# Performance work log

Hardware: AMD Instinct MI355X
Metric: run time of the kernel (lower is better)

## Reference

```python
import jax, jax.numpy as jnp
import numpy as np

N_NODES = 50000
N_EDGES = 1600000
HID = 128
NF = 128
NG = 50
NL = 6
CUTOFF = 20.0
NSEG = 64


def _ssp(x):
    # ShiftedSoftplus: softplus(x) - log(2)
    return jax.nn.softplus(x) - jnp.log(2.0).astype(x.dtype)


def setup_inputs() -> dict:
    key = jax.random.key(0)
    ks = jax.random.split(key, 24)
    s = 0.05
    inp = {
        "h": jax.random.normal(ks[0], (N_NODES, HID), dtype=jnp.float32),
        "pos": jax.random.normal(ks[1], (N_NODES, 3), dtype=jnp.float32),
        "edge_index": jax.random.randint(ks[2], (2, N_EDGES), 0, N_NODES, dtype=jnp.int64),
        "batch": jnp.sort(jax.random.randint(ks[3], (N_NODES,), 0, NSEG, dtype=jnp.int64)),
        # per-interaction-block params, stacked over NL layers (weights in [in, out] layout)
        "mlp_w1": jax.random.normal(ks[4], (NL, NG, NF), dtype=jnp.float32) * s,
        "mlp_b1": jnp.zeros((NL, NF), dtype=jnp.float32),
        "mlp_w2": jax.random.normal(ks[5], (NL, NF, NF), dtype=jnp.float32) * s,
        "mlp_b2": jnp.zeros((NL, NF), dtype=jnp.float32),
        "conv_lin1_w": jax.random.normal(ks[6], (NL, HID, NF), dtype=jnp.float32) * s,  # no bias
        "conv_lin2_w": jax.random.normal(ks[7], (NL, NF, HID), dtype=jnp.float32) * s,
        "conv_lin2_b": jnp.zeros((NL, HID), dtype=jnp.float32),
        "lin_w": jax.random.normal(ks[8], (NL, HID, HID), dtype=jnp.float32) * s,
        "lin_b": jnp.zeros((NL, HID), dtype=jnp.float32),
        # readout head
        "out1_w": jax.random.normal(ks[9], (HID, HID // 2), dtype=jnp.float32) * s,
        "out1_b": jnp.zeros((HID // 2,), dtype=jnp.float32),
        "out2_w": jax.random.normal(ks[10], (HID // 2, 1), dtype=jnp.float32) * s,
        "out2_b": jnp.zeros((1,), dtype=jnp.float32),
    }
    return inp


def reference(h, pos, edge_index, batch, mlp_w1, mlp_b1, mlp_w2, mlp_b2,
              conv_lin1_w, conv_lin2_w, conv_lin2_b, lin_w, lin_b,
              out1_w, out1_b, out2_w, out2_b):
    src = edge_index[0]  # j (messages gathered here)
    dst = edge_index[1]  # i (messages aggregated here)
    n = h.shape[0]

    # edge distances from positions (RadiusInteractionGraph.forward)
    diff = pos[src] - pos[dst]                       # [E, 3]
    d = jnp.sqrt(jnp.sum(diff * diff, axis=-1))      # [E]

    # GaussianSmearing
    offset = jnp.linspace(0.0, CUTOFF, NG, dtype=h.dtype)
    coeff = -0.5 / (offset[1] - offset[0]) ** 2
    edge_attr = jnp.exp(coeff * (d[:, None] - offset[None, :]) ** 2)  # [E, NG]

    # cosine cutoff envelope
    C = 0.5 * (jnp.cos(d * jnp.pi / CUTOFF) + 1.0)   # [E]

    for l in range(NL):
        # continuous filter from edge features
        W = _ssp(edge_attr @ mlp_w1[l] + mlp_b1[l]) @ mlp_w2[l] + mlp_b2[l]  # [E, NF]
        W = W * C[:, None]
        # CFConv: lin1 -> gather x_j -> * W -> scatter-add -> lin2
        hx = h @ conv_lin1_w[l]                       # [N, NF]
        msg = hx[src] * W                             # [E, NF]
        agg = jax.ops.segment_sum(msg, dst, num_segments=n)  # [N, NF]
        hc = agg @ conv_lin2_w[l] + conv_lin2_b[l]    # [N, HID]
        # InteractionBlock: act then lin, residual add in SchNet.forward
        h = h + (_ssp(hc) @ lin_w[l] + lin_b[l])

    # readout head
    o = _ssp(h @ out1_w + out1_b) @ out2_w + out2_b   # [N, 1]
    # 'add' readout over molecules
    return jax.ops.segment_sum(o, batch, num_segments=NSEG)  # [NSEG, 1]
```

## Files before the change

kernel.cpp:

```cpp
#include <hip/hip_runtime.h>
#include <math.h>

#define N_NODES 50000
#define N_EDGES 1600000
#define HID 128
#define NF 128
#define NG 50
#define NL 6
#define NSEG 64
#define TAB2 4096
#define CUTOFF 20.0f
#define LOG2F_ 0.6931471805599453f

typedef unsigned short u16;
typedef __attribute__((ext_vector_type(8))) short short8;
typedef __attribute__((ext_vector_type(8))) unsigned short ushort8;
typedef __attribute__((ext_vector_type(4))) float f32x4;

__device__ __forceinline__ float ssp(float x){
  float sp = fmaxf(x, 0.f) + log1pf(expf(-fabsf(x)));
  return sp - LOG2F_;
}
__device__ __forceinline__ float b2f(u16 u){
  unsigned v = ((unsigned)u) << 16; float f; __builtin_memcpy(&f, &v, 4); return f;
}
__device__ __forceinline__ u16 f2b(float f){
  unsigned u; __builtin_memcpy(&u, &f, 4);
  u += 0x7FFFu + ((u >> 16) & 1u);
  return (u16)(u >> 16);
}
__device__ __forceinline__ int swz(int row, int colb){
  return row*256 + (colb ^ ((row & 15) << 4));
}

__global__ __launch_bounds__(256) void k_hist(const int* __restrict__ ei_dst,
                                              int* __restrict__ deg){
  int e4 = blockIdx.x*blockDim.x + threadIdx.x;
  if (e4 < N_EDGES/4){
    int4 d = ((const int4*)ei_dst)[e4];
    atomicAdd(&deg[d.x], 1);
    atomicAdd(&deg[d.y], 1);
    atomicAdd(&deg[d.z], 1);
    atomicAdd(&deg[d.w], 1);
  }
}

__global__ __launch_bounds__(1024) void k_scan1(const int* __restrict__ deg,
                                                int* __restrict__ row_start,
                                                int* __restrict__ bsum){
  int i = blockIdx.x*1024 + threadIdx.x;
  int lane = threadIdx.x & 63, w = threadIdx.x >> 6;
  int x = (i < N_NODES) ? deg[i] : 0;
  int v = x;
  #pragma unroll
  for (int off = 1; off < 64; off <<= 1){
    int t = __shfl_up(v, off);
    if (lane >= off) v += t;
  }
  __shared__ int ws[16];
  if (lane == 63) ws[w] = v;
  __syncthreads();
  if (w == 0 && lane < 16){
    int t = ws[lane];
    #pragma unroll
    for (int off = 1; off < 16; off <<= 1){
      int u = __shfl_up(t, off);
      if (lane >= off) t += u;
    }
    ws[lane] = t;
  }
  __syncthreads();
  int woff = (w > 0) ? ws[w-1] : 0;
  if (i < N_NODES) row_start[i] = woff + v - x;
  if (threadIdx.x == 1023) bsum[blockIdx.x] = woff + v;
}

__global__ __launch_bounds__(1024) void k_scan2(const int* __restrict__ bsum,
                                                int* __restrict__ row_start){
  __shared__ int boff_s;
  if (threadIdx.x < 64){
    int lane = threadIdx.x;
    int acc = 0;
    for (int b = lane; b < blockIdx.x; b += 64) acc += bsum[b];
    #pragma unroll
    for (int off = 32; off >= 1; off >>= 1) acc += __shfl_xor(acc, off);
    if (lane == 0) boff_s = acc;
  }
  __syncthreads();
  int i = blockIdx.x*1024 + threadIdx.x;
  if (i < N_NODES) row_start[i] += boff_s;
  if (i == 0) row_start[N_NODES] = N_EDGES;
}

__global__ __launch_bounds__(256) void k_scatter(const int* __restrict__ ei,
                                                 const float* __restrict__ pos,
                                                 const int* __restrict__ row_start,
                                                 int* __restrict__ cursor,
                                                 unsigned* __restrict__ csr_pack){
  const float INV_STEP = (TAB2 - 1) / CUTOFF;
  for (int e = blockIdx.x*blockDim.x + threadIdx.x; e < N_EDGES; e += gridDim.x*blockDim.x){
    int s = ei[e], t = ei[N_EDGES + e];
    float dx = pos[3*s]   - pos[3*t];
    float dy = pos[3*s+1] - pos[3*t+1];
    float dz = pos[3*s+2] - pos[3*t+2];
    float d = sqrtf(dx*dx + dy*dy + dz*dz);
    int j = (int)(d * INV_STEP + 0.5f);
    if (j > TAB2 - 1) j = TAB2 - 1;
    int slot = atomicAdd(&cursor[t], 1);
    int p = row_start[t] + slot;
    __builtin_nontemporal_store(((unsigned)j << 16) | (unsigned)s, &csr_pack[p]);
  }
}

__global__ __launch_bounds__(128) void k_table(const float* __restrict__ w1, const float* __restrict__ b1,
                                               const float* __restrict__ w2, const float* __restrict__ b2,
                                               u16* __restrict__ tab){
  int l = blockIdx.x / TAB2, j = blockIdx.x % TAB2;
  int tid = threadIdx.x;
  float d = j * (CUTOFF / (TAB2 - 1));
  __shared__ float ea[NG];
  __shared__ float sbuf[NF];
  if (tid < NG){
    const float gstep = CUTOFF / (NG - 1);
    const float coeff = -0.5f / (gstep * gstep);
    float u = d - tid * gstep;
    ea[tid] = expf(coeff * u * u);
  }
  __syncthreads();
  float z = b1[l*NF + tid];
  for (int k = 0; k < NG; k++) z += ea[k] * w1[(l*NG + k)*NF + tid];
  sbuf[tid] = ssp(z);
  __syncthreads();
  float W = b2[l*NF + tid];
  for (int k = 0; k < NF; k++) W += sbuf[k] * w2[(l*NF + k)*NF + tid];
  float C = 0.5f * (cosf(d * (float)M_PI / CUTOFF) + 1.f);
  tab[((size_t)l*TAB2 + j)*NF + tid] = f2b(W * C);
}

__global__ __launch_bounds__(128) void k_wconv(const float* __restrict__ w, u16* __restrict__ wT){
  int m = blockIdx.x >> 7, o = blockIdx.x & 127;
  int i = threadIdx.x;
  wT[((size_t)m*128 + o)*128 + i] = f2b(w[((size_t)m*128 + i)*128 + o]);
}
__global__ __launch_bounds__(128) void k_wconv64(const float* __restrict__ w, u16* __restrict__ wT){
  int o = blockIdx.x;
  int i = threadIdx.x;
  wT[o*128 + i] = f2b(w[i*64 + o]);
}

__global__ __launch_bounds__(256) void k_lin1m(const float* __restrict__ h,
                                               const u16* __restrict__ w1T,
                                               u16* __restrict__ hxb){
  int tid = threadIdx.x;
  int wv = tid >> 6, l = tid & 63;
  int n0 = blockIdx.x * 64 + wv * 16;
  if (n0 >= N_NODES) return;
  int li = l & 15, lh = l >> 4;
  __shared__ u16 tiles[4][16*128];
  char* tb = (char*)&tiles[wv][0];

  short8 a[4];
  #pragma unroll
  for (int kc = 0; kc < 4; kc++){
    const float* p = &h[(size_t)(n0 + li)*HID + kc*32 + lh*8];
    union { short8 v; u16 u[8]; } t;
    #pragma unroll
    for (int e = 0; e < 8; e++) t.u[e] = f2b(p[e]);
    a[kc] = t.v;
  }
  #pragma unroll
  for (int fc = 0; fc < 8; fc++){
    f32x4 acc = {0.f,0.f,0.f,0.f};
    #pragma unroll
    for (int kc = 0; kc < 4; kc++){
      short8 b = *(const short8*)&w1T[(size_t)(fc*16 + li)*HID + kc*32 + lh*8];
      acc = __builtin_amdgcn_mfma_f32_16x16x32_bf16(a[kc], b, acc, 0, 0, 0);
    }
    #pragma unroll
    for (int r = 0; r < 4; r++)
      *(u16*)(tb + swz(lh*4 + r, fc*32 + li*2)) = f2b(acc[r]);
  }
  #pragma unroll
  for (int g = 0; g < 4; g++){
    int row = g*4 + lh;
    short8 v = *(const short8*)(tb + swz(row, li*16));
    *(short8*)&hxb[(size_t)(n0 + row)*NF + li*8] = v;
  }
}

__global__ __launch_bounds__(256) void k_edgeagg(const int* __restrict__ row_start,
                                                 const unsigned* __restrict__ csr_pack,
                                                 const u16* __restrict__ tab_l,
                                                 const u16* __restrict__ hxb,
                                                 u16* __restrict__ aggb){
  int wave = threadIdx.x >> 6, lane = threadIdx.x & 63;
  int i = blockIdx.x * 4 + wave;
  int li = lane & 15, g = lane >> 4;
  int rs = row_start[i], re = row_start[i + 1];
  float acc0[8], acc1[8];
  #pragma unroll
  for (int r = 0; r < 8; r++){ acc0[r] = 0.f; acc1[r] = 0.f; }
  for (int p = rs + g; p < re; p += 8){
    int p1 = p + 4;
    bool ok1 = p1 < re;
    unsigned v0 = csr_pack[p];
    unsigned v1 = ok1 ? csr_pack[p1] : 0u;
    int s0 = (int)(v0 & 0xFFFFu), j0 = (int)(v0 >> 16);
    ushort8 hv0 = *(const ushort8*)&hxb[(size_t)s0 * NF + li*8];
    ushort8 wv0 = *(const ushort8*)&tab_l[(size_t)j0 * NF + li*8];
    if (ok1){
      int s1 = (int)(v1 & 0xFFFFu), j1 = (int)(v1 >> 16);
      ushort8 hv1 = *(const ushort8*)&hxb[(size_t)s1 * NF + li*8];
      ushort8 wv1 = *(const ushort8*)&tab_l[(size_t)j1 * NF + li*8];
      #pragma unroll
      for (int r = 0; r < 8; r++)
        acc1[r] += b2f(hv1[r]) * b2f(wv1[r]);
    }
    #pragma unroll
    for (int r = 0; r < 8; r++)
      acc0[r] += b2f(hv0[r]) * b2f(wv0[r]);
  }
  #pragma unroll
  for (int r = 0; r < 8; r++){
    float a = acc0[r] + acc1[r];
    a += __shfl_xor(a, 16);
    a += __shfl_xor(a, 32);
    acc0[r] = a;
  }
  if (g == 0){
    union { short8 v; u16 u[8]; } o;
    #pragma unroll
    for (int r = 0; r < 8; r++) o.u[r] = f2b(acc0[r]);
    *(short8*)&aggb[(size_t)i * NF + li*8] = o.v;
  }
}

__global__ __launch_bounds__(256) void k_nodefuse(const u16* __restrict__ aggb,
                                                  const u16* __restrict__ w2T, const float* __restrict__ b2b,
                                                  const u16* __restrict__ lT,  const float* __restrict__ linb,
                                                  float* __restrict__ h,
                                                  const u16* __restrict__ w1nT,
                                                  u16* __restrict__ hxb){
  int tid = threadIdx.x;
  int wv = tid >> 6, l = tid & 63;
  int n0 = blockIdx.x * 64 + wv * 16;
  if (n0 >= N_NODES) return;
  int li = l & 15, lh = l >> 4;
  __shared__ u16 tiles[4][16*128];
  char* tb = (char*)&tiles[wv][0];

  short8 a[4];
  #pragma unroll
  for (int kc = 0; kc < 4; kc++)
    a[kc] = *(const short8*)&aggb[(size_t)(n0 + li)*NF + kc*32 + lh*8];

  #pragma unroll
  for (int fc = 0; fc < 8; fc++){
    f32x4 acc = {0.f,0.f,0.f,0.f};
    #pragma unroll
    for (int kc = 0; kc < 4; kc++){
      short8 b = *(const short8*)&w2T[(size_t)(fc*16 + li)*NF + kc*32 + lh*8];
      acc = __builtin_amdgcn_mfma_f32_16x16x32_bf16(a[kc], b, acc, 0, 0, 0);
    }
    float bias = b2b[fc*16 + li];
    #pragma unroll
    for (int r = 0; r < 4; r++){
      float s = ssp(acc[r] + bias);
      *(u16*)(tb + swz(lh*4 + r, fc*32 + li*2)) = f2b(s);
    }
  }

  short8 a2[4];
  #pragma unroll
  for (int kc = 0; kc < 4; kc++)
    a2[kc] = *(const short8*)(tb + swz(li, kc*64 + lh*16));

  #pragma unroll
  for (int fc = 0; fc < 8; fc++){
    f32x4 acc = {0.f,0.f,0.f,0.f};
    #pragma unroll
    for (int kc = 0; kc < 4; kc++){
      short8 b = *(const short8*)&lT[(size_t)(fc*16 + li)*HID + kc*32 + lh*8];
      acc = __builtin_amdgcn_mfma_f32_16x16x32_bf16(a2[kc], b, acc, 0, 0, 0);
    }
    float bias = linb[fc*16 + li];
    #pragma unroll
    for (int r = 0; r < 4; r++){
      int i = lh*4 + r;
      size_t off = (size_t)(n0 + i)*HID + fc*16 + li;
      float hn = h[off] + acc[r] + bias;
      h[off] = hn;
      if (w1nT) *(u16*)(tb + swz(i, fc*32 + li*2)) = f2b(hn);
    }
  }
  if (!w1nT) return;

  short8 a3[4];
  #pragma unroll
  for (int kc = 0; kc < 4; kc++)
    a3[kc] = *(const short8*)(tb + swz(li, kc*64 + lh*16));
  #pragma unroll
  for (int fc = 0; fc < 8; fc++){
    f32x4 acc = {0.f,0.f,0.f,0.f};
    #pragma unroll
    for (int kc = 0; kc < 4; kc++){
      short8 b = *(const short8*)&w1nT[(size_t)(fc*16 + li)*HID + kc*32 + lh*8];
      acc = __builtin_amdgcn_mfma_f32_16x16x32_bf16(a3[kc], b, acc, 0, 0, 0);
    }
    #pragma unroll
    for (int r = 0; r < 4; r++)
      *(u16*)(tb + swz(lh*4 + r, fc*32 + li*2)) = f2b(acc[r]);
  }
  #pragma unroll
  for (int g = 0; g < 4; g++){
    int row = g*4 + lh;
    short8 v = *(const short8*)(tb + swz(row, li*16));
    *(short8*)&hxb[(size_t)(n0 + row)*NF + li*8] = v;
  }
}

__global__ __launch_bounds__(256) void k_out(const float* __restrict__ h,
                                             const u16* __restrict__ o1wT, const float* __restrict__ b1,
                                             const float* __restrict__ w2, const float* __restrict__ b2,
                                             const int* __restrict__ batch, float* __restrict__ out){
  int tid = threadIdx.x;
  int wv = tid >> 6, l = tid & 63;
  int base = blockIdx.x * 64 + wv * 16;
  if (base >= N_NODES) return;
  int li = l & 15, lh = l >> 4;
  __shared__ float o_s[4][16];

  short8 a[4];
  #pragma unroll
  for (int kc = 0; kc < 4; kc++){
    const float* p = &h[(size_t)(base + li)*HID + kc*32 + lh*8];
    union { short8 v; u16 u[8]; } t;
    #pragma unroll
    for (int e = 0; e < 8; e++) t.u[e] = f2b(p[e]);
    a[kc] = t.v;
  }
  float psum[4] = {0.f,0.f,0.f,0.f};
  #pragma unroll
  for (int fc = 0; fc < 4; fc++){
    f32x4 acc = {0.f,0.f,0.f,0.f};
    #pragma unroll
    for (int kc = 0; kc < 4; kc++){
      short8 b = *(const short8*)&o1wT[(size_t)(fc*16 + li)*HID + kc*32 + lh*8];
      acc = __builtin_amdgcn_mfma_f32_16x16x32_bf16(a[kc], b, acc, 0, 0, 0);
    }
    int col = fc*16 + li;
    float bias = b1[col], w2v = w2[col];
    #pragma unroll
    for (int r = 0; r < 4; r++)
      psum[r] += ssp(acc[r] + bias) * w2v;
  }
  #pragma unroll
  for (int r = 0; r < 4; r++){
    psum[r] += __shfl_xor(psum[r], 1);
    psum[r] += __shfl_xor(psum[r], 2);
    psum[r] += __shfl_xor(psum[r], 4);
    psum[r] += __shfl_xor(psum[r], 8);
  }
  float b2v = b2[0];
  if (li == 0){
    #pragma unroll
    for (int r = 0; r < 4; r++) o_s[wv][lh*4 + r] = psum[r] + b2v;
  }
  float v = o_s[wv][li];
  int n2 = base + li;
  int seg = batch[n2];
  int segn = (li < 15) ? batch[n2 + 1] : -1;
  #pragma unroll
  for (int off = 1; off <= 8; off <<= 1){
    float vv = __shfl_up(v, off);
    int   ss = __shfl_up(seg, off);
    if (li >= off && ss == seg) v += vv;
  }
  if (l < 16 && (li == 15 || segn != seg)) atomicAdd(&out[seg], v);
}

extern "C" void kernel_launch(void* const* d_in, const int* in_sizes, int n_in,
                              void* d_out, int out_size, void* d_ws, size_t ws_size,
                              hipStream_t stream) {
  const float* h     = (const float*)d_in[0];
  const float* pos   = (const float*)d_in[1];
  const int*   ei    = (const int*)d_in[2];
  const int*   batch = (const int*)d_in[3];
  const float* mlp_w1 = (const float*)d_in[4];
  const float* mlp_b1 = (const float*)d_in[5];
  const float* mlp_w2 = (const float*)d_in[6];
  const float* mlp_b2 = (const float*)d_in[7];
  const float* cl1w  = (const float*)d_in[8];
  const float* cl2w  = (const float*)d_in[9];
  const float* cl2b  = (const float*)d_in[10];
  const float* linw  = (const float*)d_in[11];
  const float* linb  = (const float*)d_in[12];
  const float* o1w   = (const float*)d_in[13];
  const float* o1b   = (const float*)d_in[14];
  const float* o2w   = (const float*)d_in[15];
  const float* o2b   = (const float*)d_in[16];
  float* out = (float*)d_out;

  char* ws = (char*)d_ws;
  size_t off = 0;
  float* h_cur = (float*)(ws + off); off += (size_t)N_NODES*HID*4;
  u16*   aggb  = (u16*)  (ws + off); off += (size_t)N_NODES*NF*2;
  u16*   hxb   = (u16*)  (ws + off); off += (size_t)N_NODES*NF*2;
  u16*   tab   = (u16*)  (ws + off); off += (size_t)NL*TAB2*NF*2;
  u16*   w1T   = (u16*)  (ws + off); off += (size_t)NL*HID*NF*2;
  u16*   w2T   = (u16*)  (ws + off); off += (size_t)NL*NF*HID*2;
  u16*   lT    = (u16*)  (ws + off); off += (size_t)NL*HID*HID*2;
  u16*   o1wT  = (u16*)  (ws + off); off += (size_t)64*HID*2;
  unsigned* csr_pack = (unsigned*)(ws + off); off += (size_t)(N_EDGES + 16)*4;
  int* deg       = (int*)(ws + off); off += (size_t)N_NODES*4;
  int* row_start = (int*)(ws + off); off += (size_t)(N_NODES + 64)*4;
  int* cursor    = (int*)(ws + off); off += (size_t)N_NODES*4;
  int* bsum      = (int*)(ws + off); off += (size_t)64*4;

  hipMemsetAsync(out, 0, NSEG*sizeof(float), stream);
  hipMemsetAsync(deg, 0, N_NODES*sizeof(int), stream);
  hipMemsetAsync(cursor, 0, N_NODES*sizeof(int), stream);
  hipMemcpyAsync(h_cur, h, (size_t)N_NODES*HID*sizeof(float), hipMemcpyDeviceToDevice, stream);

  const int NSB = (N_NODES + 1023) / 1024;
  k_hist<<<(N_EDGES/4 + 255)/256, 256, 0, stream>>>(ei + N_EDGES, deg);
  k_scan1<<<NSB, 1024, 0, stream>>>(deg, row_start, bsum);
  k_scan2<<<NSB, 1024, 0, stream>>>(bsum, row_start);
  k_scatter<<<2048, 256, 0, stream>>>(ei, pos, row_start, cursor, csr_pack);
  k_table<<<NL*TAB2, 128, 0, stream>>>(mlp_w1, mlp_b1, mlp_w2, mlp_b2, tab);
  k_wconv<<<NL*128, 128, 0, stream>>>(cl1w, w1T);
  k_wconv<<<NL*128, 128, 0, stream>>>(cl2w, w2T);
  k_wconv<<<NL*128, 128, 0, stream>>>(linw, lT);
  k_wconv64<<<64, 128, 0, stream>>>(o1w, o1wT);

  const int NBLK = (N_NODES + 63) / 64;
  k_lin1m<<<NBLK, 256, 0, stream>>>(h_cur, w1T, hxb);
  for (int l = 0; l < NL; l++){
    k_edgeagg<<<N_NODES/4, 256, 0, stream>>>(row_start, csr_pack,
                                             tab + (size_t)l*TAB2*NF, hxb, aggb);
    const u16* w1n = (l + 1 < NL) ? (w1T + (size_t)(l+1)*HID*NF) : nullptr;
    k_nodefuse<<<NBLK, 256, 0, stream>>>(aggb, w2T + (size_t)l*NF*HID, cl2b + (size_t)l*HID,
                                         lT + (size_t)l*HID*HID, linb + (size_t)l*HID,
                                         h_cur, w1n, hxb);
  }
  k_out<<<NBLK, 256, 0, stream>>>(h_cur, o1wT, o1b, o2w, o2b, batch, out);
}
```

Baseline: 937.0 us.

## Pad CSR rows to even length and load edge pairs as 64-bit in edgeagg

Each node's CSR row is padded to an even length with a sentinel entry that points at a zero-weight table row. The aggregation kernel can then fetch two packed edge indices per lane with one 64-bit nontemporal load, prefetch the next pair, and drop the per-pair bounds branch. The bf16 multiply-accumulate now works on packed 32-bit words with shifts and masks. In exchange it adds a padding kernel, a larger CSR buffer and a few wasted gathers for the padded entries.

```diff
diff --git a/kernel.cpp b/kernel.cpp
--- a/kernel.cpp
+++ b/kernel.cpp
@@ -11,8 +11,10 @@
 #define TAB2 4096
 #define CUTOFF 20.0f
 #define LOG2F_ 0.6931471805599453f
+#define SENTINEL 0x0FFF0000u
 
 typedef unsigned short u16;
+typedef unsigned long long u64;
 typedef __attribute__((ext_vector_type(8))) short short8;
 typedef __attribute__((ext_vector_type(8))) unsigned short ushort8;
 typedef __attribute__((ext_vector_type(4))) float f32x4;
@@ -28,6 +30,13 @@
   unsigned u; __builtin_memcpy(&u, &f, 4);
   u += 0x7FFFu + ((u >> 16) & 1u);
   return (u16)(u >> 16);
+}
+__device__ __forceinline__ float u2f(unsigned u){
+  float f; __builtin_memcpy(&f, &u, 4); return f;
+}
+__device__ __forceinline__ void fma2(unsigned hp, unsigned wp, float& a0, float& a1){
+  a0 = fmaf(u2f(hp << 16), u2f(wp << 16), a0);
+  a1 = fmaf(u2f(hp & 0xFFFF0000u), u2f(wp & 0xFFFF0000u), a1);
 }
 __device__ __forceinline__ int swz(int row, int colb){
   return row*256 + (colb ^ ((row & 15) << 4));
@@ -50,7 +59,7 @@
                                                 int* __restrict__ bsum){
   int i = blockIdx.x*1024 + threadIdx.x;
   int lane = threadIdx.x & 63, w = threadIdx.x >> 6;
-  int x = (i < N_NODES) ? deg[i] : 0;
+  int x = (i < N_NODES) ? ((deg[i] + 1) & ~1) : 0;
   int v = x;
   #pragma unroll
   for (int off = 1; off < 64; off <<= 1){
@@ -76,6 +85,7 @@
 }
 
 __global__ __launch_bounds__(1024) void k_scan2(const int* __restrict__ bsum,
+                                                const int* __restrict__ deg,
                                                 int* __restrict__ row_start){
   __shared__ int boff_s;
   if (threadIdx.x < 64){
@@ -88,8 +98,19 @@
   }
   __syncthreads();
   int i = blockIdx.x*1024 + threadIdx.x;
-  if (i < N_NODES) row_start[i] += boff_s;
-  if (i == 0) row_start[N_NODES] = N_EDGES;
+  if (i < N_NODES){
+    int r = row_start[i] + boff_s;
+    row_start[i] = r;
+    if (i == N_NODES - 1) row_start[N_NODES] = r + ((deg[i] + 1) & ~1);
+  }
+}
+
+__global__ __launch_bounds__(256) void k_pad(const int* __restrict__ deg,
+                                             const int* __restrict__ row_start,
+                                             unsigned* __restrict__ csr_pack){
+  int i = blockIdx.x*blockDim.x + threadIdx.x;
+  if (i < N_NODES && (deg[i] & 1))
+    csr_pack[row_start[i] + deg[i]] = SENTINEL;
 }
 
 __global__ __launch_bounds__(256) void k_scatter(const int* __restrict__ ei,
@@ -197,28 +218,51 @@
   int i = blockIdx.x * 4 + wave;
   int li = lane & 15, g = lane >> 4;
   int rs = row_start[i], re = row_start[i + 1];
+  int len = re - rs;
   float acc0[8], acc1[8];
   #pragma unroll
   for (int r = 0; r < 8; r++){ acc0[r] = 0.f; acc1[r] = 0.f; }
-  for (int p = rs + g; p < re; p += 8){
-    int p1 = p + 4;
-    bool ok1 = p1 < re;
-    unsigned v0 = csr_pack[p];
-    unsigned v1 = ok1 ? csr_pack[p1] : 0u;
+
+  int p = rs + 2*g;
+  int nmain = len >> 3;
+  u64 v = 0;
+  if (p < re) v = __builtin_nontemporal_load((const u64*)&csr_pack[p]);
+
+  for (int t = 0; t < nmain; ++t){
+    unsigned v0 = (unsigned)v, v1 = (unsigned)(v >> 32);
     int s0 = (int)(v0 & 0xFFFFu), j0 = (int)(v0 >> 16);
-    ushort8 hv0 = *(const ushort8*)&hxb[(size_t)s0 * NF + li*8];
-    ushort8 wv0 = *(const ushort8*)&tab_l[(size_t)j0 * NF + li*8];
-    if (ok1){
-      int s1 = (int)(v1 & 0xFFFFu), j1 = (int)(v1 >> 16);
-      ushort8 hv1 = *(const ushort8*)&hxb[(size_t)s1 * NF + li*8];
-      ushort8 wv1 = *(const ushort8*)&tab_l[(size_t)j1 * NF + li*8];
-      #pragma unroll
-      for (int r = 0; r < 8; r++)
-        acc1[r] += b2f(hv1[r]) * b2f(wv1[r]);
-    }
-    #pragma unroll
-    for (int r = 0; r < 8; r++)
-      acc0[r] += b2f(hv0[r]) * b2f(wv0[r]);
+    int s1 = (int)(v1 & 0xFFFFu), j1 = (int)(v1 >> 16);
+    uint4 hv0 = *(const uint4*)&hxb[(size_t)s0 * NF + li*8];
+    uint4 wv0 = *(const uint4*)&tab_l[(size_t)j0 * NF + li*8];
+    uint4 hv1 = *(const uint4*)&hxb[(size_t)s1 * NF + li*8];
+    uint4 wv1 = *(const uint4*)&tab_l[(size_t)j1 * NF + li*8];
+    u64 vn = __builtin_nontemporal_load((const u64*)&csr_pack[p + 8]);
+    fma2(hv0.x, wv0.x, acc0[0], acc0[1]);
+    fma2(hv0.y, wv0.y, acc0[2], acc0[3]);
+    fma2(hv0.z, wv0.z, acc0[4], acc0[5]);
+    fma2(hv0.w, wv0.w, acc0[6], acc0[7]);
+    fma2(hv1.x, wv1.x, acc1[0], acc1[1]);
+    fma2(hv1.y, wv1.y, acc1[2], acc1[3]);
+    fma2(hv1.z, wv1.z, acc1[4], acc1[5]);
+    fma2(hv1.w, wv1.w, acc1[6], acc1[7]);
+    v = vn; p += 8;
+  }
+  if (p < re){
+    unsigned v0 = (unsigned)v, v1 = (unsigned)(v >> 32);
+    int s0 = (int)(v0 & 0xFFFFu), j0 = (int)(v0 >> 16);
+    int s1 = (int)(v1 & 0xFFFFu), j1 = (int)(v1 >> 16);
+    uint4 hv0 = *(const uint4*)&hxb[(size_t)s0 * NF + li*8];
+    uint4 wv0 = *(const uint4*)&tab_l[(size_t)j0 * NF + li*8];
+    uint4 hv1 = *(const uint4*)&hxb[(size_t)s1 * NF + li*8];
+    uint4 wv1 = *(const uint4*)&tab_l[(size_t)j1 * NF + li*8];
+    fma2(hv0.x, wv0.x, acc0[0], acc0[1]);
+    fma2(hv0.y, wv0.y, acc0[2], acc0[3]);
+    fma2(hv0.z, wv0.z, acc0[4], acc0[5]);
+    fma2(hv0.w, wv0.w, acc0[6], acc0[7]);
+    fma2(hv1.x, wv1.x, acc1[0], acc1[1]);
+    fma2(hv1.y, wv1.y, acc1[2], acc1[3]);
+    fma2(hv1.z, wv1.z, acc1[4], acc1[5]);
+    fma2(hv1.w, wv1.w, acc1[6], acc1[7]);
   }
   #pragma unroll
   for (int r = 0; r < 8; r++){
@@ -411,7 +455,7 @@
   u16*   w2T   = (u16*)  (ws + off); off += (size_t)NL*NF*HID*2;
   u16*   lT    = (u16*)  (ws + off); off += (size_t)NL*HID*HID*2;
   u16*   o1wT  = (u16*)  (ws + off); off += (size_t)64*HID*2;
-  unsigned* csr_pack = (unsigned*)(ws + off); off += (size_t)(N_EDGES + 16)*4;
+  unsigned* csr_pack = (unsigned*)(ws + off); off += (size_t)(N_EDGES + N_NODES + 32)*4;
   int* deg       = (int*)(ws + off); off += (size_t)N_NODES*4;
   int* row_start = (int*)(ws + off); off += (size_t)(N_NODES + 64)*4;
   int* cursor    = (int*)(ws + off); off += (size_t)N_NODES*4;
@@ -425,8 +469,9 @@
   const int NSB = (N_NODES + 1023) / 1024;
   k_hist<<<(N_EDGES/4 + 255)/256, 256, 0, stream>>>(ei + N_EDGES, deg);
   k_scan1<<<NSB, 1024, 0, stream>>>(deg, row_start, bsum);
-  k_scan2<<<NSB, 1024, 0, stream>>>(bsum, row_start);
+  k_scan2<<<NSB, 1024, 0, stream>>>(bsum, deg, row_start);
   k_scatter<<<2048, 256, 0, stream>>>(ei, pos, row_start, cursor, csr_pack);
+  k_pad<<<(N_NODES + 255)/256, 256, 0, stream>>>(deg, row_start, csr_pack);
   k_table<<<NL*TAB2, 128, 0, stream>>>(mlp_w1, mlp_b1, mlp_w2, mlp_b2, tab);
   k_wconv<<<NL*128, 128, 0, stream>>>(cl1w, w1T);
   k_wconv<<<NL*128, 128, 0, stream>>>(cl2w, w2T);
```

New measurement: 971.8 us. 1.04x slower.

## Build filter lookup table with bf16 MFMA instead of scalar FP32 loops

Applied to the files above, without the earlier changes.

Replaces the per-entry scalar table kernel (one block per distance sample, 128 threads doing serial dot products) with an MFMA-based kernel that computes 16 table rows per wave via two bf16 matrix multiplies, staging the intermediate softplus activations in swizzled LDS. It adds small conversion kernels that transpose and pad the MLP weights to bf16. This is meant to cut the cost of the table precompute (24k blocks with serial FP32 loops). In exchange, the first layer's Gaussian features and the hidden activations are rounded to bf16, which slightly lowers the table's precision.

```diff
diff --git a/kernel.cpp b/kernel.cpp
--- a/kernel.cpp
+++ b/kernel.cpp
@@ -13,6 +13,7 @@
 #define LOG2F_ 0.6931471805599453f
 
 typedef unsigned short u16;
+typedef unsigned long long u64;
 typedef __attribute__((ext_vector_type(8))) short short8;
 typedef __attribute__((ext_vector_type(8))) unsigned short ushort8;
 typedef __attribute__((ext_vector_type(4))) float f32x4;
@@ -112,31 +113,6 @@
   }
 }
 
-__global__ __launch_bounds__(128) void k_table(const float* __restrict__ w1, const float* __restrict__ b1,
-                                               const float* __restrict__ w2, const float* __restrict__ b2,
-                                               u16* __restrict__ tab){
-  int l = blockIdx.x / TAB2, j = blockIdx.x % TAB2;
-  int tid = threadIdx.x;
-  float d = j * (CUTOFF / (TAB2 - 1));
-  __shared__ float ea[NG];
-  __shared__ float sbuf[NF];
-  if (tid < NG){
-    const float gstep = CUTOFF / (NG - 1);
-    const float coeff = -0.5f / (gstep * gstep);
-    float u = d - tid * gstep;
-    ea[tid] = expf(coeff * u * u);
-  }
-  __syncthreads();
-  float z = b1[l*NF + tid];
-  for (int k = 0; k < NG; k++) z += ea[k] * w1[(l*NG + k)*NF + tid];
-  sbuf[tid] = ssp(z);
-  __syncthreads();
-  float W = b2[l*NF + tid];
-  for (int k = 0; k < NF; k++) W += sbuf[k] * w2[(l*NF + k)*NF + tid];
-  float C = 0.5f * (cosf(d * (float)M_PI / CUTOFF) + 1.f);
-  tab[((size_t)l*TAB2 + j)*NF + tid] = f2b(W * C);
-}
-
 __global__ __launch_bounds__(128) void k_wconv(const float* __restrict__ w, u16* __restrict__ wT){
   int m = blockIdx.x >> 7, o = blockIdx.x & 127;
   int i = threadIdx.x;
@@ -146,6 +122,85 @@
   int o = blockIdx.x;
   int i = threadIdx.x;
   wT[o*128 + i] = f2b(w[i*64 + o]);
+}
+__global__ __launch_bounds__(64) void k_wmlp1(const float* __restrict__ w, u16* __restrict__ wT){
+  int l = blockIdx.x >> 7, o = blockIdx.x & 127;
+  int k = threadIdx.x;
+  wT[((size_t)l*128 + o)*64 + k] = (k < NG) ? f2b(w[((size_t)l*NG + k)*NF + o]) : (u16)0;
+}
+
+__global__ __launch_bounds__(256) void k_tablem(const u16* __restrict__ w1mT,
+                                                const float* __restrict__ b1,
+                                                const u16* __restrict__ w2mT,
+                                                const float* __restrict__ b2,
+                                                u16* __restrict__ tab){
+  int tid = threadIdx.x;
+  int wv = tid >> 6, l = tid & 63;
+  int lay = blockIdx.x >> 6;
+  int j0 = ((blockIdx.x & 63) << 6) + wv*16;
+  int li = l & 15, lh = l >> 4;
+  __shared__ u16 tiles[4][16*128];
+  char* tb = (char*)&tiles[wv][0];
+
+  const float step2 = CUTOFF / (TAB2 - 1);
+  const float gstep = CUTOFF / (NG - 1);
+  const float coeff = -0.5f / (gstep*gstep);
+
+  float d = (j0 + li) * step2;
+  short8 a1[2];
+  #pragma unroll
+  for (int kc = 0; kc < 2; kc++){
+    union { short8 v; u16 u[8]; } t;
+    #pragma unroll
+    for (int e = 0; e < 8; e++){
+      int k = kc*32 + lh*8 + e;
+      float u = d - k*gstep;
+      float val = (k < NG) ? expf(coeff * u * u) : 0.f;
+      t.u[e] = f2b(val);
+    }
+    a1[kc] = t.v;
+  }
+  #pragma unroll
+  for (int fc = 0; fc < 8; fc++){
+    f32x4 acc = {0.f,0.f,0.f,0.f};
+    #pragma unroll
+    for (int kc = 0; kc < 2; kc++){
+      short8 b = *(const short8*)&w1mT[(size_t)(lay*128 + fc*16 + li)*64 + kc*32 + lh*8];
+      acc = __builtin_amdgcn_mfma_f32_16x16x32_bf16(a1[kc], b, acc, 0, 0, 0);
+    }
+    float bias = b1[lay*NF + fc*16 + li];
+    #pragma unroll
+    for (int r = 0; r < 4; r++){
+      float s = ssp(acc[r] + bias);
+      *(u16*)(tb + swz(lh*4 + r, fc*32 + li*2)) = f2b(s);
+    }
+  }
+  short8 a2[4];
+  #pragma unroll
+  for (int kc = 0; kc < 4; kc++)
+    a2[kc] = *(const short8*)(tb + swz(li, kc*64 + lh*16));
+  #pragma unroll
+  for (int fc = 0; fc < 8; fc++){
+    f32x4 acc = {0.f,0.f,0.f,0.f};
+    #pragma unroll
+    for (int kc = 0; kc < 4; kc++){
+      short8 b = *(const short8*)&w2mT[(size_t)(lay*128 + fc*16 + li)*128 + kc*32 + lh*8];
+      acc = __builtin_amdgcn_mfma_f32_16x16x32_bf16(a2[kc], b, acc, 0, 0, 0);
+    }
+    float bias = b2[lay*NF + fc*16 + li];
+    #pragma unroll
+    for (int r = 0; r < 4; r++){
+      float dr = (j0 + lh*4 + r) * step2;
+      float C = 0.5f * (cosf(dr * (float)M_PI / CUTOFF) + 1.f);
+      *(u16*)(tb + swz(lh*4 + r, fc*32 + li*2)) = f2b((acc[r] + bias) * C);
+    }
+  }
+  #pragma unroll
+  for (int g = 0; g < 4; g++){
+    int row = g*4 + lh;
+    short8 v = *(const short8*)(tb + swz(row, li*16));
+    *(short8*)&tab[((size_t)lay*TAB2 + j0 + row)*NF + li*8] = v;
+  }
 }
 
 __global__ __launch_bounds__(256) void k_lin1m(const float* __restrict__ h,
@@ -411,6 +466,8 @@
   u16*   w2T   = (u16*)  (ws + off); off += (size_t)NL*NF*HID*2;
   u16*   lT    = (u16*)  (ws + off); off += (size_t)NL*HID*HID*2;
   u16*   o1wT  = (u16*)  (ws + off); off += (size_t)64*HID*2;
+  u16*   w1mT  = (u16*)  (ws + off); off += (size_t)NL*NF*64*2;
+  u16*   w2mT  = (u16*)  (ws + off); off += (size_t)NL*NF*NF*2;
   unsigned* csr_pack = (unsigned*)(ws + off); off += (size_t)(N_EDGES + 16)*4;
   int* deg       = (int*)(ws + off); off += (size_t)N_NODES*4;
   int* row_start = (int*)(ws + off); off += (size_t)(N_NODES + 64)*4;
@@ -427,7 +484,9 @@
   k_scan1<<<NSB, 1024, 0, stream>>>(deg, row_start, bsum);
   k_scan2<<<NSB, 1024, 0, stream>>>(bsum, row_start);
   k_scatter<<<2048, 256, 0, stream>>>(ei, pos, row_start, cursor, csr_pack);
-  k_table<<<NL*TAB2, 128, 0, stream>>>(mlp_w1, mlp_b1, mlp_w2, mlp_b2, tab);
+  k_wmlp1<<<NL*128, 64, 0, stream>>>(mlp_w1, w1mT);
+  k_wconv<<<NL*128, 128, 0, stream>>>(mlp_w2, w2mT);
+  k_tablem<<<NL*64, 256, 0, stream>>>(w1mT, mlp_b1, w2mT, mlp_b2, tab);
   k_wconv<<<NL*128, 128, 0, stream>>>(cl1w, w1T);
   k_wconv<<<NL*128, 128, 0, stream>>>(cl2w, w2T);
   k_wconv<<<NL*128, 128, 0, stream>>>(linw, lT);
```

After: 889.8 us, median of 2. -5.0%, faster.
